# Kernel optimization log

Measured on AMD Instinct MI355X. Metric: run time of the kernel, lower is better.

Reference implementation:

```python
import jax, jax.numpy as jnp
import numpy as np

B = 8192      # batch
T = 8         # obs_len
E = 256       # feature_dim
M = 20        # num_modes
NH = 4        # attention heads
HD = E // NH  # head dim
FS = 12       # future_steps
LN_EPS = 1e-5


def setup_inputs() -> dict:
    key = jax.random.key(0)
    ks = jax.random.split(key, 32)
    s = 0.05
    def n(i, shape):
        return jax.random.normal(ks[i], shape, jnp.float32) * s
    return {
        "observed_trajectory": jax.random.normal(ks[0], (B, T, 2), jnp.float32),
        # 2-layer LSTM (torch gate order i,f,g,o)
        "w_ih0": n(1, (4 * E, 2)), "w_hh0": n(2, (4 * E, E)),
        "b_ih0": n(3, (4 * E,)), "b_hh0": n(4, (4 * E,)),
        "w_ih1": n(5, (4 * E, E)), "w_hh1": n(6, (4 * E, E)),
        "b_ih1": n(7, (4 * E,)), "b_hh1": n(8, (4 * E,)),
        # 20 MHA modules, weights stacked over mode axis
        "in_proj_w": n(9, (M, 3 * E, E)), "in_proj_b": n(10, (M, 3 * E)),
        "out_w": n(11, (M, E, E)), "out_b": n(12, (M, E)),
        # FFN: LN -> Linear(256,1024) -> ReLU -> Linear(1024,256) -> LN
        "ln1_g": jnp.ones((E,)), "ln1_b": jnp.zeros((E,)),
        "ffn_w1": n(13, (1024, E)), "ffn_b1": n(14, (1024,)),
        "ffn_w2": n(15, (E, 1024)), "ffn_b2": n(16, (E,)),
        "ln2_g": jnp.ones((E,)), "ln2_b": jnp.zeros((E,)),
        # decoder MLP
        "dec_w1": n(17, (512, E)), "dec_b1": n(18, (512,)),
        "dec_w2": n(19, (FS * 2, 512)), "dec_b2": n(20, (FS * 2,)),
        # scorer MLP
        "sc_w1": n(21, (128, E)), "sc_b1": n(22, (128,)),
        "sc_w2": n(23, (1, 128)), "sc_b2": n(24, (1,)),
    }


def _lstm_layer(xs, w_ih, w_hh, b_ih, b_hh):
    # xs: (T, B, in_dim) -> (ys (T,B,E), h_T (B,E))
    bb = xs.shape[1]
    h0 = jnp.zeros((bb, E), xs.dtype)
    c0 = jnp.zeros((bb, E), xs.dtype)
    def step(carry, x):
        h, c = carry
        g = x @ w_ih.T + h @ w_hh.T + b_ih + b_hh
        i, f, gg, o = jnp.split(g, 4, axis=-1)
        c = jax.nn.sigmoid(f) * c + jax.nn.sigmoid(i) * jnp.tanh(gg)
        h = jax.nn.sigmoid(o) * jnp.tanh(c)
        return (h, c), h
    (h_t, _), ys = jax.lax.scan(step, (h0, c0), xs)
    return ys, h_t


def _ln(x, g, b):
    m = jnp.mean(x, -1, keepdims=True)
    v = jnp.mean((x - m) ** 2, -1, keepdims=True)
    return (x - m) * jax.lax.rsqrt(v + LN_EPS) * g + b


def _forward(observed_trajectory, w_ih0, w_hh0, b_ih0, b_hh0,
             w_ih1, w_hh1, b_ih1, b_hh1,
             in_proj_w, in_proj_b, out_w, out_b,
             ln1_g, ln1_b, ffn_w1, ffn_b1, ffn_w2, ffn_b2, ln2_g, ln2_b,
             dec_w1, dec_b1, dec_w2, dec_b2,
             sc_w1, sc_b1, sc_w2, sc_b2):
    bsz = observed_trajectory.shape[0]
    # --- TrajectoryEncoder: 2-layer LSTM, take last-step output of layer 2 ---
    xs = jnp.transpose(observed_trajectory, (1, 0, 2))  # (T, B, 2)
    ys0, _ = _lstm_layer(xs, w_ih0, w_hh0, b_ih0, b_hh0)
    _, emb = _lstm_layer(ys0, w_ih1, w_hh1, b_ih1, b_hh1)  # (B, E)

    # --- MultiModalTransformer: 20 MHA modules on seq_len=1 (fused over modes) ---
    # query == key == value == emb. Dropout is eval-mode identity.
    qkv = jnp.einsum('be,mfe->bmf', emb, in_proj_w) + in_proj_b  # (B, M, 3E)
    q, k, v = jnp.split(qkv, 3, axis=-1)
    q = q.reshape(bsz, M, NH, HD)
    k = k.reshape(bsz, M, NH, HD)
    v = v.reshape(bsz, M, NH, HD)
    # kv length is 1 -> softmax over a single score is identically 1
    scores = jnp.sum(q * k, -1, keepdims=True) / jnp.sqrt(jnp.float32(HD))  # (B,M,NH,1)
    attn = jax.nn.softmax(scores, axis=-1)
    ctx = (attn * v).reshape(bsz, M, E)
    attn_out = jnp.einsum('bmf,mof->bmo', ctx, out_w) + out_b  # (B, M, E)
    # FFN (no residual in original module)
    h = _ln(attn_out, ln1_g, ln1_b)
    h = jax.nn.relu(h @ ffn_w1.T + ffn_b1)
    h = h @ ffn_w2.T + ffn_b2
    mm_emb = _ln(h, ln2_g, ln2_b)  # (B, M, E)

    # --- TrajectoryDecoder ---
    last_pos = observed_trajectory[:, -1, :]  # (B, 2)
    d = jax.nn.elu(mm_emb @ dec_w1.T + dec_b1)
    deltas = (d @ dec_w2.T + dec_b2).reshape(bsz, M, FS, 2)
    predictions = deltas + last_pos[:, None, None, :]

    # --- ModeScorer ---
    s = jax.nn.elu(mm_emb @ sc_w1.T + sc_b1)
    scores_out = (s @ sc_w2.T + sc_b2)[..., 0]  # (B, M)
    return predictions, scores_out


def reference(observed_trajectory, w_ih0, w_hh0, b_ih0, b_hh0,
              w_ih1, w_hh1, b_ih1, b_hh1,
              in_proj_w, in_proj_b, out_w, out_b,
              ln1_g, ln1_b, ffn_w1, ffn_b1, ffn_w2, ffn_b2, ln2_g, ln2_b,
              dec_w1, dec_b1, dec_w2, dec_b2,
              sc_w1, sc_b1, sc_w2, sc_b2):
    return _forward(observed_trajectory, w_ih0, w_hh0, b_ih0, b_hh0,
                    w_ih1, w_hh1, b_ih1, b_hh1,
                    in_proj_w, in_proj_b, out_w, out_b,
                    ln1_g, ln1_b, ffn_w1, ffn_b1, ffn_w2, ffn_b2, ln2_g, ln2_b,
                    dec_w1, dec_b1, dec_w2, dec_b2,
                    sc_w1, sc_b1, sc_w2, sc_b2)
```

## Files before the change

### kernel.cpp

```cpp
#include <hip/hip_runtime.h>
#include <math.h>


typedef float4 f4;
typedef unsigned int u32;
typedef unsigned short u16;
typedef __attribute__((ext_vector_type(16))) float f32x16;
typedef __attribute__((ext_vector_type(8)))  short s16x8;

__device__ __forceinline__ float sigm(float x){ return 1.0f/(1.0f + __expf(-x)); }
__device__ __forceinline__ float tanhfast(float x){ return 2.0f*sigm(2.0f*x) - 1.0f; }
__device__ __forceinline__ float eluf(float x){ return x > 0.f ? x : expm1f(x); }
__device__ __forceinline__ u16 f2bf(float x){
  u32 u = __float_as_uint(x);
  return (u16)((u + 0x7FFFu + ((u>>16)&1u)) >> 16);
}
__device__ __forceinline__ float bf2f(u16 h){ return __uint_as_float(((u32)h)<<16); }


#define LSTR 264

__global__ __launch_bounds__(256, 4)
void w2c_kernel(const float* __restrict__ out_w, const float* __restrict__ ipw,
                float* __restrict__ W2c)
{
  __shared__ float As[16][68];
  __shared__ float Bs2[16][68];
  const int tid = threadIdx.x;
  const int m = blockIdx.y;
  const int o0 = (blockIdx.x >> 2) * 64, e0 = (blockIdx.x & 3) * 64;
  const int trow = tid >> 4, tcol = tid & 15;
  const float* Ap = out_w + (size_t)m * 65536;
  const float* Bp = ipw + ((size_t)m * 768 + 512) * 256;
  float acc[16];
#pragma unroll
  for (int z = 0; z < 16; ++z) acc[z] = 0.f;
  for (int kb = 0; kb < 256; kb += 16) {
    { int row = tid >> 2, ko = (tid & 3) * 4;
      f4 v = *(const f4*)(Ap + (size_t)(o0+row)*256 + kb + ko);
      As[ko+0][row]=v.x; As[ko+1][row]=v.y; As[ko+2][row]=v.z; As[ko+3][row]=v.w; }
    { int k = tid >> 4, eo = (tid & 15) * 4;
      *(f4*)&Bs2[k][eo] = *(const f4*)(Bp + (size_t)(kb+k)*256 + e0 + eo); }
    __syncthreads();
#pragma unroll
    for (int k = 0; k < 16; ++k) {
      f4 a4 = *(const f4*)&As[k][trow*4];
      f4 b4 = *(const f4*)&Bs2[k][tcol*4];
      acc[0]+=a4.x*b4.x; acc[1]+=a4.x*b4.y; acc[2]+=a4.x*b4.z; acc[3]+=a4.x*b4.w;
      acc[4]+=a4.y*b4.x; acc[5]+=a4.y*b4.y; acc[6]+=a4.y*b4.z; acc[7]+=a4.y*b4.w;
      acc[8]+=a4.z*b4.x; acc[9]+=a4.z*b4.y; acc[10]+=a4.z*b4.z; acc[11]+=a4.z*b4.w;
      acc[12]+=a4.w*b4.x; acc[13]+=a4.w*b4.y; acc[14]+=a4.w*b4.z; acc[15]+=a4.w*b4.w;
    }
    __syncthreads();
  }
#pragma unroll
  for (int i = 0; i < 4; ++i)
    *(f4*)&W2c[((size_t)m*256 + o0 + trow*4 + i)*256 + e0 + tcol*4] =
        make_float4(acc[i*4+0], acc[i*4+1], acc[i*4+2], acc[i*4+3]);
}

__global__ void b2c_kernel(const float* __restrict__ out_w, const float* __restrict__ out_b,
                           const float* __restrict__ ipb, float* __restrict__ b2c)
{
  __shared__ float pb[256];
  const int m = blockIdx.x, o = threadIdx.x;
  pb[o] = ipb[(size_t)m*768 + 512 + o];
  __syncthreads();
  const float* wr = out_w + ((size_t)m*256 + o)*256;
  float acc = out_b[(size_t)m*256 + o];
  for (int f = 0; f < 256; f += 4) {
    f4 w = *(const f4*)&wr[f];
    acc += w.x*pb[f] + w.y*pb[f+1] + w.z*pb[f+2] + w.w*pb[f+3];
  }
  b2c[(size_t)m*256 + o] = acc;
}

__device__ __forceinline__ void cvt_seg(const float* __restrict__ src, u16* __restrict__ dst,
                                        int Creal, int lognks, int g)
{
  const int l = g & 63;
  const int cks = g >> 6;
  const int ks = cks & ((1 << lognks) - 1);
  const int ct = cks >> lognks;
  const int c = ct*32 + (l & 31);
  const int K = 16 << lognks;
  const int k = ks*16 + ((l >> 5) * 8);
  s16x8 r;
  if (c < Creal) {
    const float* s = src + (size_t)c * K + k;
    f4 v0 = *(const f4*)s;
    f4 v1 = *(const f4*)(s + 4);
    r[0]=(short)f2bf(v0.x); r[1]=(short)f2bf(v0.y); r[2]=(short)f2bf(v0.z); r[3]=(short)f2bf(v0.w);
    r[4]=(short)f2bf(v1.x); r[5]=(short)f2bf(v1.y); r[6]=(short)f2bf(v1.z); r[7]=(short)f2bf(v1.w);
  } else {
#pragma unroll
    for (int j = 0; j < 8; ++j) r[j] = 0;
  }
  *(s16x8*)(dst + (size_t)g * 8) = r;
}

__global__ __launch_bounds__(256)
void wcvt_all(const float* __restrict__ whh0, const float* __restrict__ wih1,
              const float* __restrict__ whh1, const float* __restrict__ W2c,
              const float* __restrict__ ffn1, const float* __restrict__ ffn2,
              const float* __restrict__ dec1, const float* __restrict__ dec2,
              const float* __restrict__ sc1,  u16* __restrict__ dst)
{
  int g = blockIdx.x * 256 + threadIdx.x;
  if      (g <  32768) cvt_seg(whh0, dst + 0,       1024, 4, g);
  else if (g <  65536) cvt_seg(wih1, dst + 262144,  1024, 4, g - 32768);
  else if (g <  98304) cvt_seg(whh1, dst + 524288,  1024, 4, g - 65536);
  else if (g < 262144) cvt_seg(W2c,  dst + 786432,  5120, 4, g - 98304);
  else if (g < 294912) cvt_seg(ffn1, dst + 2097152, 1024, 4, g - 262144);
  else if (g < 327680) cvt_seg(ffn2, dst + 2359296,  256, 6, g - 294912);
  else if (g < 344064) cvt_seg(dec1, dst + 2621440,  512, 4, g - 327680);
  else if (g < 346112) cvt_seg(dec2, dst + 2752512,   24, 5, g - 344064);
  else if (g < 350208) cvt_seg(sc1,  dst + 2768896,  128, 4, g - 346112);
}

__global__ __launch_bounds__(512, 2)
void lstm_fused(const u16* __restrict__ whh0f, const u16* __restrict__ wih1f,
                const u16* __restrict__ whh1f, const float* __restrict__ w_ih0,
                const float* __restrict__ b_ih0, const float* __restrict__ b_hh0,
                const float* __restrict__ b_ih1, const float* __restrict__ b_hh1,
                const float* __restrict__ obs, u16* __restrict__ emb)
{
  __shared__ u16 h0s[32 * LSTR];
  __shared__ u16 h1s[32 * LSTR];
  __shared__ float obs_s[512];
  const int tid = threadIdx.x;
  const int lane = tid & 63, w = tid >> 6;
  const int col = lane & 31, hi = lane >> 5;
  const int r0 = blockIdx.x * 32;
  if (tid < 512) obs_s[tid] = obs[(size_t)r0 * 16 + tid];

  float bs0[4], bs1[4], xw0[4], xw1[4];
#pragma unroll
  for (int g = 0; g < 4; ++g) {
    const int cg = g*256 + w*32 + col;
    bs0[g] = b_ih0[cg] + b_hh0[cg];
    bs1[g] = b_ih1[cg] + b_hh1[cg];
    xw0[g] = w_ih0[2*cg];
    xw1[g] = w_ih0[2*cg + 1];
  }
  float c0v[16], c1v[16];
#pragma unroll
  for (int r = 0; r < 16; ++r) { c0v[r] = 0.f; c1v[r] = 0.f; }

  f32x16 za;
#pragma unroll
  for (int i = 0; i < 16; ++i) za[i] = 0.f;

  __syncthreads();

  for (int t = 0; t < 8; ++t) {
    f32x16 accA[4], accB[4];
#pragma unroll
    for (int g = 0; g < 4; ++g) { accA[g] = za; accB[g] = za; }
    if (t > 0) {
#pragma unroll 2
      for (int ks = 0; ks < 16; ++ks) {
        s16x8 a0 = *(const s16x8*)(h0s + col*LSTR + ks*16 + hi*8);
        s16x8 a1 = *(const s16x8*)(h1s + col*LSTR + ks*16 + hi*8);
#pragma unroll
        for (int g = 0; g < 4; ++g) {
          const size_t fo = ((size_t)((g*8 + w)*16 + ks)*64 + lane)*8;
          s16x8 bA = *(const s16x8*)(whh0f + fo);
          accA[g] = __builtin_amdgcn_mfma_f32_32x32x16_bf16(a0, bA, accA[g], 0, 0, 0);
          s16x8 bB = *(const s16x8*)(whh1f + fo);
          accB[g] = __builtin_amdgcn_mfma_f32_32x32x16_bf16(a1, bB, accB[g], 0, 0, 0);
        }
      }
    }
    __syncthreads();
#pragma unroll
    for (int r = 0; r < 16; ++r) {
      const int row = (r&3) + 8*(r>>2) + 4*hi;
      const float x0 = obs_s[row*16 + 2*t], x1 = obs_s[row*16 + 2*t + 1];
      const float gi = accA[0][r] + bs0[0] + x0*xw0[0] + x1*xw1[0];
      const float gf = accA[1][r] + bs0[1] + x0*xw0[1] + x1*xw1[1];
      const float gg = accA[2][r] + bs0[2] + x0*xw0[2] + x1*xw1[2];
      const float go = accA[3][r] + bs0[3] + x0*xw0[3] + x1*xw1[3];
      const float cn = sigm(gf)*c0v[r] + sigm(gi)*tanhfast(gg);
      c0v[r] = cn;
      h0s[row*LSTR + w*32 + col] = f2bf(sigm(go)*tanhfast(cn));
    }
    __syncthreads();
#pragma unroll 2
    for (int ks = 0; ks < 16; ++ks) {
      s16x8 a = *(const s16x8*)(h0s + col*LSTR + ks*16 + hi*8);
#pragma unroll
      for (int g = 0; g < 4; ++g) {
        s16x8 b = *(const s16x8*)(wih1f + ((size_t)((g*8 + w)*16 + ks)*64 + lane)*8);
        accB[g] = __builtin_amdgcn_mfma_f32_32x32x16_bf16(a, b, accB[g], 0, 0, 0);
      }
    }
#pragma unroll
    for (int r = 0; r < 16; ++r) {
      const int row = (r&3) + 8*(r>>2) + 4*hi;
      const float gi = accB[0][r] + bs1[0];
      const float gf = accB[1][r] + bs1[1];
      const float gg = accB[2][r] + bs1[2];
      const float go = accB[3][r] + bs1[3];
      const float cn = sigm(gf)*c1v[r] + sigm(gi)*tanhfast(gg);
      c1v[r] = cn;
      h1s[row*LSTR + w*32 + col] = f2bf(sigm(go)*tanhfast(cn));
    }
    __syncthreads();
  }
#pragma unroll
  for (int kk = 0; kk < 2; ++kk) {
    const int gi2 = tid + kk*512;
    const int row = gi2 >> 5, grp = gi2 & 31;
    *(s16x8*)(emb + (size_t)(r0 + row)*256 + grp*8) = *(const s16x8*)(h1s + row*LSTR + grp*8);
  }
}

__device__ __forceinline__ void gemm128(const u16* As, const u16* __restrict__ Bf,
                                        f32x16 acc[4], int w, int lane)
{
  const int col = lane & 31, hi = lane >> 5;
#pragma unroll 4
  for (int ks = 0; ks < 16; ++ks) {
    s16x8 b = *(const s16x8*)(Bf + ((size_t)(w*16 + ks)*64 + lane)*8);
#pragma unroll
    for (int i = 0; i < 4; ++i) {
      s16x8 a = *(const s16x8*)(As + (i*32 + col)*LSTR + ks*16 + hi*8);
      acc[i] = __builtin_amdgcn_mfma_f32_32x32x16_bf16(a, b, acc[i], 0, 0, 0);
    }
  }
}

__device__ __forceinline__ void gemm_ffn2_128(const u16* As, const u16* __restrict__ Bf,
                                              f32x16 acc[4], int c4, int w, int lane)
{
  const int col = lane & 31, hi = lane >> 5;
#pragma unroll 4
  for (int ks = 0; ks < 16; ++ks) {
    s16x8 b = *(const s16x8*)(Bf + ((size_t)(w*64 + c4*16 + ks)*64 + lane)*8);
#pragma unroll
    for (int i = 0; i < 4; ++i) {
      s16x8 a = *(const s16x8*)(As + (i*32 + col)*LSTR + ks*16 + hi*8);
      acc[i] = __builtin_amdgcn_mfma_f32_32x32x16_bf16(a, b, acc[i], 0, 0, 0);
    }
  }
}

template<int ACT>
__device__ __forceinline__ void epi_store128(f32x16 acc[4], const float* __restrict__ bias,
                                             u16* Ys, int w, int lane)
{
  const int col = lane & 31, hi = lane >> 5, cg = w*32 + col;
  const float bv = bias[cg];
#pragma unroll
  for (int i = 0; i < 4; ++i)
#pragma unroll
    for (int r = 0; r < 16; ++r) {
      float v = acc[i][r] + bv;
      if (ACT == 1) v = fmaxf(v, 0.f);
      else if (ACT == 2) v = eluf(v);
      const int row = i*32 + (r&3) + 8*(r>>2) + 4*hi;
      Ys[row*LSTR + cg] = f2bf(v);
    }
}

__device__ __forceinline__ void lnpass128(const u16* In, u16* Out,
    const float* __restrict__ g, const float* __restrict__ b, int tid)
{
  const int lane = tid & 63, w = tid >> 6;
  f4 gv = *(const f4*)&g[lane*4];
  f4 bv = *(const f4*)&b[lane*4];
#pragma unroll
  for (int i = 0; i < 16; ++i) {
    const int row = w*16 + i;
    ushort4 uv = *(const ushort4*)(In + row*LSTR + lane*4);
    float v0 = bf2f(uv.x), v1 = bf2f(uv.y), v2 = bf2f(uv.z), v3 = bf2f(uv.w);
    float s  = v0 + v1 + v2 + v3;
    float ss = v0*v0 + v1*v1 + v2*v2 + v3*v3;
#pragma unroll
    for (int d = 1; d < 64; d <<= 1) { s += __shfl_xor(s, d); ss += __shfl_xor(ss, d); }
    const float mean = s * (1.f/256.f);
    const float rs = rsqrtf(ss * (1.f/256.f) - mean*mean + 1e-5f);
    ushort4 o;
    o.x = f2bf((v0 - mean)*rs*gv.x + bv.x);
    o.y = f2bf((v1 - mean)*rs*gv.y + bv.y);
    o.z = f2bf((v2 - mean)*rs*gv.z + bv.z);
    o.w = f2bf((v3 - mean)*rs*gv.w + bv.w);
    *(ushort4*)(Out + row*LSTR + lane*4) = o;
  }
}

__global__ __launch_bounds__(512, 2)
void mode_stack(const u16* __restrict__ emb, const u16* __restrict__ W2cf,
  const float* __restrict__ b2c,
  const float* __restrict__ ln1_g, const float* __restrict__ ln1_b,
  const u16* __restrict__ ffn1f, const float* __restrict__ ffn_b1,
  const u16* __restrict__ ffn2f, const float* __restrict__ ffn_b2,
  const float* __restrict__ ln2_g, const float* __restrict__ ln2_b,
  const u16* __restrict__ dec1f, const float* __restrict__ dec_b1,
  const u16* __restrict__ dec2f, const float* __restrict__ dec_b2,
  const u16* __restrict__ sc1f,  const float* __restrict__ sc_b1,
  const float* __restrict__ sc_w2, const float* __restrict__ sc_b2,
  const float* __restrict__ obs, float* __restrict__ pred, float* __restrict__ score)
{
  __shared__ u16 Xs[128 * LSTR];
  __shared__ u16 Ys[128 * LSTR];
  __shared__ float obs_ls[256];
  const int tid = threadIdx.x;
  const int lane = tid & 63, w = tid >> 6;
  const int col = lane & 31, hi = lane >> 5;
  const int r0 = blockIdx.x * 128;
  const int m  = blockIdx.y;

  f32x16 za;
#pragma unroll
  for (int i = 0; i < 16; ++i) za[i] = 0.f;

#pragma unroll
  for (int kk = 0; kk < 8; ++kk) {
    const int gi2 = tid + kk*512;
    const int row = gi2 >> 5, grp = gi2 & 31;
    *(s16x8*)(Xs + row*LSTR + grp*8) = *(const s16x8*)(emb + (size_t)(r0 + row)*256 + grp*8);
  }
  if (tid < 256) obs_ls[tid] = obs[(size_t)(r0 + (tid >> 1))*16 + 14 + (tid & 1)];
  __syncthreads();

  {
    f32x16 acc[4];
#pragma unroll
    for (int i = 0; i < 4; ++i) acc[i] = za;
    gemm128(Xs, W2cf + (size_t)m*65536, acc, w, lane);
    epi_store128<0>(acc, b2c + m*256, Ys, w, lane);
  }
  __syncthreads();
  lnpass128(Ys, Xs, ln1_g, ln1_b, tid);
  __syncthreads();

  f32x16 h2[4];
#pragma unroll
  for (int i = 0; i < 4; ++i) h2[i] = za;
  for (int c4 = 0; c4 < 4; ++c4) {
    f32x16 tacc[4];
#pragma unroll
    for (int i = 0; i < 4; ++i) tacc[i] = za;
    gemm128(Xs, ffn1f + (size_t)c4*65536, tacc, w, lane);
    epi_store128<1>(tacc, ffn_b1 + c4*256, Ys, w, lane);
    __syncthreads();
    gemm_ffn2_128(Ys, ffn2f, h2, c4, w, lane);
    __syncthreads();
  }
  epi_store128<0>(h2, ffn_b2, Ys, w, lane);
  __syncthreads();
  lnpass128(Ys, Xs, ln2_g, ln2_b, tid);
  __syncthreads();

  f32x16 dv[4];
#pragma unroll
  for (int i = 0; i < 4; ++i) dv[i] = za;
  for (int c2 = 0; c2 < 2; ++c2) {
    f32x16 tacc[4];
#pragma unroll
    for (int i = 0; i < 4; ++i) tacc[i] = za;
    gemm128(Xs, dec1f + (size_t)c2*65536, tacc, w, lane);
    epi_store128<2>(tacc, dec_b1 + c2*256, Ys, w, lane);
    __syncthreads();
    if (w == 0) {
#pragma unroll 4
      for (int ks = 0; ks < 16; ++ks) {
        s16x8 b = *(const s16x8*)(dec2f + ((size_t)(c2*16 + ks)*64 + lane)*8);
#pragma unroll
        for (int i = 0; i < 4; ++i) {
          s16x8 a = *(const s16x8*)(Ys + (i*32 + col)*LSTR + ks*16 + hi*8);
          dv[i] = __builtin_amdgcn_mfma_f32_32x32x16_bf16(a, b, dv[i], 0, 0, 0);
        }
      }
    }
    __syncthreads();
  }
  if (w == 0 && col < 24) {
    const float db = dec_b2[col];
#pragma unroll
    for (int i = 0; i < 4; ++i)
#pragma unroll
      for (int r = 0; r < 16; ++r) {
        const int row = i*32 + (r&3) + 8*(r>>2) + 4*hi;
        const float lp = obs_ls[row*2 + (col & 1)];
        pred[((size_t)(r0 + row)*20 + m)*24 + col] = dv[i][r] + db + lp;
      }
  }

  if (w < 4) {
    f32x16 sacc[4];
#pragma unroll
    for (int i = 0; i < 4; ++i) sacc[i] = za;
    gemm128(Xs, sc1f, sacc, w, lane);
    epi_store128<2>(sacc, sc_b1, Ys, w, lane);
  }
  __syncthreads();
  {
    const float scb2 = sc_b2[0];
    const float2 w2v = *(const float2*)&sc_w2[lane*2];
#pragma unroll
    for (int i = 0; i < 16; ++i) {
      const int row = w*16 + i;
      u32 pv = *(const u32*)(Ys + row*LSTR + lane*2);
      float part = bf2f((u16)(pv & 0xFFFF))*w2v.x + bf2f((u16)(pv >> 16))*w2v.y;
#pragma unroll
      for (int d = 1; d < 64; d <<= 1) part += __shfl_xor(part, d);
      if (lane == 0) score[(size_t)(r0 + row)*20 + m] = part + scb2;
    }
  }
}

extern "C" void kernel_launch(void* const* d_in, const int* in_sizes, int n_in,
                              void* d_out, int out_size, void* d_ws, size_t ws_size,
                              hipStream_t stream)
{
  (void)in_sizes; (void)n_in; (void)out_size; (void)ws_size;
  const float* obs    = (const float*)d_in[0];
  const float* w_ih0  = (const float*)d_in[1];
  const float* w_hh0  = (const float*)d_in[2];
  const float* b_ih0  = (const float*)d_in[3];
  const float* b_hh0  = (const float*)d_in[4];
  const float* w_ih1  = (const float*)d_in[5];
  const float* w_hh1  = (const float*)d_in[6];
  const float* b_ih1  = (const float*)d_in[7];
  const float* b_hh1  = (const float*)d_in[8];
  const float* ipw    = (const float*)d_in[9];
  const float* ipb    = (const float*)d_in[10];
  const float* out_w  = (const float*)d_in[11];
  const float* out_b  = (const float*)d_in[12];
  const float* ln1_g  = (const float*)d_in[13];
  const float* ln1_b  = (const float*)d_in[14];
  const float* ffn_w1 = (const float*)d_in[15];
  const float* ffn_b1 = (const float*)d_in[16];
  const float* ffn_w2 = (const float*)d_in[17];
  const float* ffn_b2 = (const float*)d_in[18];
  const float* ln2_g  = (const float*)d_in[19];
  const float* ln2_b  = (const float*)d_in[20];
  const float* dec_w1 = (const float*)d_in[21];
  const float* dec_b1 = (const float*)d_in[22];
  const float* dec_w2 = (const float*)d_in[23];
  const float* dec_b2 = (const float*)d_in[24];
  const float* sc_w1  = (const float*)d_in[25];
  const float* sc_b1  = (const float*)d_in[26];
  const float* sc_w2  = (const float*)d_in[27];
  const float* sc_b2  = (const float*)d_in[28];

  float* outp   = (float*)d_out;
  float* pred   = outp;
  float* scoreo = outp + (size_t)8192*20*24;

  float* wsf   = (float*)d_ws;
  float* W2c   = wsf;
  float* b2cp  = wsf + 1310720;
  u16*   wsh   = (u16*)(wsf + 1315840);
  u16* whh0f = wsh + 0;
  u16* wih1f = wsh + 262144;
  u16* whh1f = wsh + 524288;
  u16* W2cf  = wsh + 786432;
  u16* ffn1f = wsh + 2097152;
  u16* ffn2f = wsh + 2359296;
  u16* dec1f = wsh + 2621440;
  u16* dec2f = wsh + 2752512;
  u16* sc1f  = wsh + 2768896;
  u16* emb   = wsh + 2801664;

  w2c_kernel<<<dim3(16, 20), 256, 0, stream>>>(out_w, ipw, W2c);
  b2c_kernel<<<20, 256, 0, stream>>>(out_w, out_b, ipb, b2cp);
  wcvt_all<<<1368, 256, 0, stream>>>(w_hh0, w_ih1, w_hh1, W2c, ffn_w1, ffn_w2,
                                     dec_w1, dec_w2, sc_w1, wsh);
  lstm_fused<<<256, 512, 0, stream>>>(whh0f, wih1f, whh1f, w_ih0, b_ih0, b_hh0,
                                      b_ih1, b_hh1, obs, emb);
  mode_stack<<<dim3(64, 20), 512, 0, stream>>>(emb, W2cf, b2cp,
      ln1_g, ln1_b, ffn1f, ffn_b1, ffn2f, ffn_b2, ln2_g, ln2_b,
      dec1f, dec_b1, dec2f, dec_b2, sc1f, sc_b1, sc_w2, sc_b2,
      obs, pred, scoreo);
}
```

Measured before the change: 847.9 us.

## Split mode_stack tiles across 16 waves with 1024-thread blocks

Doubles the mode_stack block from 8 to 16 waves. Each wave now owns one 32-column tile and half of the 128 rows, so it keeps 2 accumulators instead of 4. The aim is more waves to hide latency and less register pressure per wave. In exchange, each B fragment is loaded twice (once per row half), and the LDS footprint per block may limit how many blocks fit on a CU. The LSTM layer-1 input GEMM loop is also unrolled 4 instead of 2.

```diff
diff --git a/kernel.cpp b/kernel.cpp
--- a/kernel.cpp
+++ b/kernel.cpp
@@ -186,7 +186,7 @@
       h0s[row*LSTR + w*32 + col] = f2bf(sigm(go)*tanhfast(cn));
     }
     __syncthreads();
-#pragma unroll 2
+#pragma unroll 4
     for (int ks = 0; ks < 16; ++ks) {
       s16x8 a = *(const s16x8*)(h0s + col*LSTR + ks*16 + hi*8);
 #pragma unroll
@@ -217,49 +217,49 @@
 }
 
 __device__ __forceinline__ void gemm128(const u16* As, const u16* __restrict__ Bf,
-                                        f32x16 acc[4], int w, int lane)
+                                        f32x16 acc[2], int ct, int rh, int lane)
 {
   const int col = lane & 31, hi = lane >> 5;
 #pragma unroll 4
   for (int ks = 0; ks < 16; ++ks) {
-    s16x8 b = *(const s16x8*)(Bf + ((size_t)(w*16 + ks)*64 + lane)*8);
-#pragma unroll
-    for (int i = 0; i < 4; ++i) {
-      s16x8 a = *(const s16x8*)(As + (i*32 + col)*LSTR + ks*16 + hi*8);
+    s16x8 b = *(const s16x8*)(Bf + ((size_t)(ct*16 + ks)*64 + lane)*8);
+#pragma unroll
+    for (int i = 0; i < 2; ++i) {
+      s16x8 a = *(const s16x8*)(As + ((rh*2 + i)*32 + col)*LSTR + ks*16 + hi*8);
       acc[i] = __builtin_amdgcn_mfma_f32_32x32x16_bf16(a, b, acc[i], 0, 0, 0);
     }
   }
 }
 
 __device__ __forceinline__ void gemm_ffn2_128(const u16* As, const u16* __restrict__ Bf,
-                                              f32x16 acc[4], int c4, int w, int lane)
+                                              f32x16 acc[2], int c4, int ct, int rh, int lane)
 {
   const int col = lane & 31, hi = lane >> 5;
 #pragma unroll 4
   for (int ks = 0; ks < 16; ++ks) {
-    s16x8 b = *(const s16x8*)(Bf + ((size_t)(w*64 + c4*16 + ks)*64 + lane)*8);
-#pragma unroll
-    for (int i = 0; i < 4; ++i) {
-      s16x8 a = *(const s16x8*)(As + (i*32 + col)*LSTR + ks*16 + hi*8);
+    s16x8 b = *(const s16x8*)(Bf + ((size_t)(ct*64 + c4*16 + ks)*64 + lane)*8);
+#pragma unroll
+    for (int i = 0; i < 2; ++i) {
+      s16x8 a = *(const s16x8*)(As + ((rh*2 + i)*32 + col)*LSTR + ks*16 + hi*8);
       acc[i] = __builtin_amdgcn_mfma_f32_32x32x16_bf16(a, b, acc[i], 0, 0, 0);
     }
   }
 }
 
 template<int ACT>
-__device__ __forceinline__ void epi_store128(f32x16 acc[4], const float* __restrict__ bias,
-                                             u16* Ys, int w, int lane)
-{
-  const int col = lane & 31, hi = lane >> 5, cg = w*32 + col;
+__device__ __forceinline__ void epi_store128(f32x16 acc[2], const float* __restrict__ bias,
+                                             u16* Ys, int ct, int rh, int lane)
+{
+  const int col = lane & 31, hi = lane >> 5, cg = ct*32 + col;
   const float bv = bias[cg];
 #pragma unroll
-  for (int i = 0; i < 4; ++i)
+  for (int i = 0; i < 2; ++i)
 #pragma unroll
     for (int r = 0; r < 16; ++r) {
       float v = acc[i][r] + bv;
       if (ACT == 1) v = fmaxf(v, 0.f);
       else if (ACT == 2) v = eluf(v);
-      const int row = i*32 + (r&3) + 8*(r>>2) + 4*hi;
+      const int row = (rh*2 + i)*32 + (r&3) + 8*(r>>2) + 4*hi;
       Ys[row*LSTR + cg] = f2bf(v);
     }
 }
@@ -271,8 +271,8 @@
   f4 gv = *(const f4*)&g[lane*4];
   f4 bv = *(const f4*)&b[lane*4];
 #pragma unroll
-  for (int i = 0; i < 16; ++i) {
-    const int row = w*16 + i;
+  for (int i = 0; i < 8; ++i) {
+    const int row = w*8 + i;
     ushort4 uv = *(const ushort4*)(In + row*LSTR + lane*4);
     float v0 = bf2f(uv.x), v1 = bf2f(uv.y), v2 = bf2f(uv.z), v3 = bf2f(uv.w);
     float s  = v0 + v1 + v2 + v3;
@@ -290,7 +290,7 @@
   }
 }
 
-__global__ __launch_bounds__(512, 2)
+__global__ __launch_bounds__(1024, 4)
 void mode_stack(const u16* __restrict__ emb, const u16* __restrict__ W2cf,
   const float* __restrict__ b2c,
   const float* __restrict__ ln1_g, const float* __restrict__ ln1_b,
@@ -308,6 +308,7 @@
   __shared__ float obs_ls[256];
   const int tid = threadIdx.x;
   const int lane = tid & 63, w = tid >> 6;
+  const int ct = w & 7, rh = w >> 3;
   const int col = lane & 31, hi = lane >> 5;
   const int r0 = blockIdx.x * 128;
   const int m  = blockIdx.y;
@@ -317,8 +318,8 @@
   for (int i = 0; i < 16; ++i) za[i] = 0.f;
 
 #pragma unroll
-  for (int kk = 0; kk < 8; ++kk) {
-    const int gi2 = tid + kk*512;
+  for (int kk = 0; kk < 4; ++kk) {
+    const int gi2 = tid + kk*1024;
     const int row = gi2 >> 5, grp = gi2 & 31;
     *(s16x8*)(Xs + row*LSTR + grp*8) = *(const s16x8*)(emb + (size_t)(r0 + row)*256 + grp*8);
   }
@@ -326,83 +327,71 @@
   __syncthreads();
 
   {
-    f32x16 acc[4];
-#pragma unroll
-    for (int i = 0; i < 4; ++i) acc[i] = za;
-    gemm128(Xs, W2cf + (size_t)m*65536, acc, w, lane);
-    epi_store128<0>(acc, b2c + m*256, Ys, w, lane);
+    f32x16 acc[2]; acc[0] = za; acc[1] = za;
+    gemm128(Xs, W2cf + (size_t)m*65536, acc, ct, rh, lane);
+    epi_store128<0>(acc, b2c + m*256, Ys, ct, rh, lane);
   }
   __syncthreads();
   lnpass128(Ys, Xs, ln1_g, ln1_b, tid);
   __syncthreads();
 
-  f32x16 h2[4];
-#pragma unroll
-  for (int i = 0; i < 4; ++i) h2[i] = za;
+  f32x16 h2[2]; h2[0] = za; h2[1] = za;
   for (int c4 = 0; c4 < 4; ++c4) {
-    f32x16 tacc[4];
-#pragma unroll
-    for (int i = 0; i < 4; ++i) tacc[i] = za;
-    gemm128(Xs, ffn1f + (size_t)c4*65536, tacc, w, lane);
-    epi_store128<1>(tacc, ffn_b1 + c4*256, Ys, w, lane);
-    __syncthreads();
-    gemm_ffn2_128(Ys, ffn2f, h2, c4, w, lane);
-    __syncthreads();
-  }
-  epi_store128<0>(h2, ffn_b2, Ys, w, lane);
+    f32x16 tacc[2]; tacc[0] = za; tacc[1] = za;
+    gemm128(Xs, ffn1f + (size_t)c4*65536, tacc, ct, rh, lane);
+    epi_store128<1>(tacc, ffn_b1 + c4*256, Ys, ct, rh, lane);
+    __syncthreads();
+    gemm_ffn2_128(Ys, ffn2f, h2, c4, ct, rh, lane);
+    __syncthreads();
+  }
+  epi_store128<0>(h2, ffn_b2, Ys, ct, rh, lane);
   __syncthreads();
   lnpass128(Ys, Xs, ln2_g, ln2_b, tid);
   __syncthreads();
 
-  f32x16 dv[4];
-#pragma unroll
-  for (int i = 0; i < 4; ++i) dv[i] = za;
+  f32x16 dv[2]; dv[0] = za; dv[1] = za;
   for (int c2 = 0; c2 < 2; ++c2) {
-    f32x16 tacc[4];
-#pragma unroll
-    for (int i = 0; i < 4; ++i) tacc[i] = za;
-    gemm128(Xs, dec1f + (size_t)c2*65536, tacc, w, lane);
-    epi_store128<2>(tacc, dec_b1 + c2*256, Ys, w, lane);
-    __syncthreads();
-    if (w == 0) {
+    f32x16 tacc[2]; tacc[0] = za; tacc[1] = za;
+    gemm128(Xs, dec1f + (size_t)c2*65536, tacc, ct, rh, lane);
+    epi_store128<2>(tacc, dec_b1 + c2*256, Ys, ct, rh, lane);
+    __syncthreads();
+    if (ct == 0) {
 #pragma unroll 4
       for (int ks = 0; ks < 16; ++ks) {
         s16x8 b = *(const s16x8*)(dec2f + ((size_t)(c2*16 + ks)*64 + lane)*8);
 #pragma unroll
-        for (int i = 0; i < 4; ++i) {
-          s16x8 a = *(const s16x8*)(Ys + (i*32 + col)*LSTR + ks*16 + hi*8);
+        for (int i = 0; i < 2; ++i) {
+          s16x8 a = *(const s16x8*)(Ys + ((rh*2 + i)*32 + col)*LSTR + ks*16 + hi*8);
           dv[i] = __builtin_amdgcn_mfma_f32_32x32x16_bf16(a, b, dv[i], 0, 0, 0);
         }
       }
     }
     __syncthreads();
   }
-  if (w == 0 && col < 24) {
+  if (ct == 0 && col < 24) {
     const float db = dec_b2[col];
 #pragma unroll
-    for (int i = 0; i < 4; ++i)
+    for (int i = 0; i < 2; ++i)
 #pragma unroll
       for (int r = 0; r < 16; ++r) {
-        const int row = i*32 + (r&3) + 8*(r>>2) + 4*hi;
+        const int row = (rh*2 + i)*32 + (r&3) + 8*(r>>2) + 4*hi;
         const float lp = obs_ls[row*2 + (col & 1)];
         pred[((size_t)(r0 + row)*20 + m)*24 + col] = dv[i][r] + db + lp;
       }
   }
 
-  if (w < 4) {
-    f32x16 sacc[4];
-#pragma unroll
-    for (int i = 0; i < 4; ++i) sacc[i] = za;
-    gemm128(Xs, sc1f, sacc, w, lane);
-    epi_store128<2>(sacc, sc_b1, Ys, w, lane);
+  if (ct < 4) {
+    f32x16 sacc[2]; sacc[0] = za; sacc[1] = za;
+    gemm128(Xs, sc1f, sacc, ct, rh, lane);
+    epi_store128<2>(sacc, sc_b1, Ys, ct, rh, lane);
   }
   __syncthreads();
   {
     const float scb2 = sc_b2[0];
     const float2 w2v = *(const float2*)&sc_w2[lane*2];
 #pragma unroll
-    for (int i = 0; i < 16; ++i) {
-      const int row = w*16 + i;
+    for (int i = 0; i < 8; ++i) {
+      const int row = w*8 + i;
       u32 pv = *(const u32*)(Ys + row*LSTR + lane*2);
       float part = bf2f((u16)(pv & 0xFFFF))*w2v.x + bf2f((u16)(pv >> 16))*w2v.y;
 #pragma unroll
@@ -472,7 +461,7 @@
                                      dec_w1, dec_w2, sc_w1, wsh);
   lstm_fused<<<256, 512, 0, stream>>>(whh0f, wih1f, whh1f, w_ih0, b_ih0, b_hh0,
                                       b_ih1, b_hh1, obs, emb);
-  mode_stack<<<dim3(64, 20), 512, 0, stream>>>(emb, W2cf, b2cp,
+  mode_stack<<<dim3(64, 20), 1024, 0, stream>>>(emb, W2cf, b2cp,
       ln1_g, ln1_b, ffn1f, ffn_b1, ffn2f, ffn_b2, ln2_g, ln2_b,
       dec1f, dec_b1, dec2f, dec_b2, sc1f, sc_b1, sc_w2, sc_b2,
       obs, pred, scoreo);
```

Measured after the change: 811.3 us. 1.05x faster.
